# Kernel optimization log

Measured on AMD Instinct MI355X. Metric: run time of the kernel, lower is better.

## Reference

```python
import jax, jax.numpy as jnp
import numpy as np

DELTA_SCALE = 0.99
DELTA_MIN = 0.01


def setup_inputs() -> dict:
    key = jax.random.key(0)
    ks = jax.random.split(key, 6)
    B, S, Dm, N = 8, 4096, 1024, 16
    x = jax.random.normal(ks[0], (B, S, Dm), dtype=jnp.float32)
    A = jax.random.normal(ks[1], (N,), dtype=jnp.float32) * 0.1 - 1.0
    W_b = jax.random.normal(ks[2], (N, Dm), dtype=jnp.float32) / np.sqrt(Dm)
    b_b = jnp.zeros((N,), dtype=jnp.float32)
    W_c = jax.random.normal(ks[3], (Dm, N), dtype=jnp.float32) / np.sqrt(N)
    b_c = jnp.zeros((Dm,), dtype=jnp.float32)
    D = jnp.ones((Dm,), dtype=jnp.float32)
    W_t = jax.random.normal(ks[4], (1, Dm), dtype=jnp.float32) / np.sqrt(Dm)
    b_t = jnp.zeros((1,), dtype=jnp.float32)
    W_o = jax.random.normal(ks[5], (Dm, Dm), dtype=jnp.float32) / np.sqrt(Dm)
    b_o = jnp.zeros((Dm,), dtype=jnp.float32)
    return {"x": x, "A": A, "W_b": W_b, "b_b": b_b, "W_c": W_c, "b_c": b_c,
            "D": D, "W_t": W_t, "b_t": b_t, "W_o": W_o, "b_o": b_o}


def _scan_combine(left, right):
    # h_t = a_t * h_{t-1} + b_t ; compose two affine maps
    a_l, u_l = left
    a_r, u_r = right
    return (a_l * a_r, a_r * u_l + u_r)


def reference(x, A, W_b, b_b, W_c, b_c, D, W_t, b_t, W_o, b_o):
    # x: [B, S, Dm]
    delta = jax.nn.sigmoid(jnp.einsum('bsd,od->bso', x, W_t) + b_t)  # [B,S,1]
    delta = delta * DELTA_SCALE + DELTA_MIN
    Bu = jnp.einsum('bsd,nd->bsn', x, W_b) + b_b                     # [B,S,N]
    A_exp = jnp.exp(A[None, None, :] * delta)                        # [B,S,N]
    # Parallel associative scan over time: h_t = A_exp_t * h_{t-1} + Bu_t
    _, h = jax.lax.associative_scan(_scan_combine, (A_exp, Bu), axis=1)
    outputs = jnp.einsum('bsn,dn->bsd', h, W_c) + b_c                # [B,S,Dm]
    y = outputs + x * D[None, None, :]
    y = jnp.einsum('bsd,od->bso', y, W_o) + b_o                      # dropout = eval identity
    return y
```

## Files before the change

kernel.cpp:

```cpp
#include <hip/hip_runtime.h>
#include <hip/hip_bf16.h>
#include <cstdint>
#include <cstddef>

#define B_SZ 8
#define S_SZ 4096
#define DM   1024
#define NS   16
#define M_SZ (B_SZ * S_SZ)

typedef __attribute__((ext_vector_type(4))) float f32x4;
typedef __attribute__((ext_vector_type(8))) short short8;
typedef __attribute__((ext_vector_type(4))) unsigned short ushort4v;

__device__ __forceinline__ unsigned short f2bf(float f) {
  unsigned u = __float_as_uint(f);
  u += 0x7fffu + ((u >> 16) & 1u);
  return (unsigned short)(u >> 16);
}

__global__ __launch_bounds__(256) void k0_prep(
    const float* __restrict__ Wo, const float* __restrict__ D,
    const float* __restrict__ Wc, const float* __restrict__ bc,
    const float* __restrict__ bo, unsigned short* __restrict__ WoD16,
    unsigned short* __restrict__ Wco16, float* __restrict__ bz) {
  const int o = blockIdx.x;
  const int t = threadIdx.x;
  const float* wor = Wo + (size_t)o * DM;

  f32x4 wv = *(const f32x4*)(wor + t * 4);
  f32x4 dv = *(const f32x4*)(D + t * 4);
  ushort4v u;
#pragma unroll
  for (int i = 0; i < 4; ++i) u[i] = f2bf(wv[i] * dv[i]);
  *(ushort4v*)(WoD16 + (size_t)o * DM + t * 4) = u;

  const int n = t & 15, ds = t >> 4;
  float s = 0.f;
  const float* wod = wor + ds * 64;
  const float* wcd = Wc + (size_t)(ds * 64) * NS + n;
#pragma unroll 8
  for (int j = 0; j < 64; ++j) s += wod[j] * wcd[j * NS];

  f32x4 bcv = *(const f32x4*)(bc + t * 4);
  float pb = wv[0] * bcv[0] + wv[1] * bcv[1] + wv[2] * bcv[2] + wv[3] * bcv[3];

  __shared__ float red[16][17];
  __shared__ float redb[256];
  red[n][ds] = s;
  redb[t] = pb;
  __syncthreads();
  if (t < 16) {
    float acc = 0.f;
#pragma unroll
    for (int k = 0; k < 16; ++k) acc += red[t][k];
    Wco16[(size_t)o * 32 + t] = f2bf(acc);
    Wco16[(size_t)o * 32 + 16 + t] = 0;
  }
  if (t == 0) {
    float b = bo[o];
    for (int i = 0; i < 256; ++i) b += redb[i];
    bz[o] = b;
  }
}

__global__ __launch_bounds__(256) void k1_proj(
    const float* __restrict__ x, const float* __restrict__ A,
    const float* __restrict__ Wb, const float* __restrict__ bb,
    const float* __restrict__ Wt, const float* __restrict__ bt,
    float* __restrict__ Ae, float* __restrict__ Bu,
    unsigned short* __restrict__ x16) {
  __shared__ __align__(16) float Wb_s[NS * DM];
  __shared__ __align__(16) float Wt_s[DM];
  __shared__ __align__(16) float Bu_s[NS][64];
  __shared__ __align__(16) float Ae_s[NS][64];

  const int tid = threadIdx.x;
#pragma unroll
  for (int i = 0; i < 16; ++i) {
    int fi = tid * 4 + i * 1024;
    *(f32x4*)(Wb_s + fi) = *(const f32x4*)(Wb + fi);
  }
  *(f32x4*)(Wt_s + tid * 4) = *(const f32x4*)(Wt + tid * 4);

  const int lane = tid & 63;
  const int w = tid >> 6;
  const int p = lane & 15;
  const int g = lane >> 4;
  const int nlane = ((lane & 1) << 3) | (((lane >> 1) & 1) << 2) |
                    (((lane >> 2) & 1) << 1) | ((lane >> 3) & 1);
  const float a_n = A[nlane];
  const float bb_n = bb[nlane];
  const float bt0 = bt[0];

  __syncthreads();

  const int m0 = blockIdx.x * 64;
  const int b_idx = m0 >> 12;
  const int s0 = m0 & (S_SZ - 1);
  const int dq = g * 64 + p * 4;

#pragma unroll 1
  for (int grp = 0; grp < 4; ++grp) {
    const int rbase = w * 16 + grp * 4;
    f32x4 xr[4][4];
#pragma unroll
    for (int rr = 0; rr < 4; ++rr) {
      const int m = m0 + rbase + rr;
      const float* xp = x + (size_t)m * DM;
#pragma unroll
      for (int q = 0; q < 4; ++q) {
        xr[rr][q] = *(const f32x4*)(xp + q * 256 + dq);
        ushort4v xu;
#pragma unroll
        for (int e = 0; e < 4; ++e) xu[e] = f2bf(xr[rr][q][e]);
        *(ushort4v*)(x16 + (size_t)m * DM + q * 256 + dq) = xu;
      }
    }
    float bu[16][4];
#pragma unroll
    for (int n = 0; n < 16; ++n)
#pragma unroll
      for (int rr = 0; rr < 4; ++rr) bu[n][rr] = 0.f;
    float da[4] = {0.f, 0.f, 0.f, 0.f};

#pragma unroll
    for (int n = 0; n < 16; ++n) {
#pragma unroll
      for (int q = 0; q < 4; ++q) {
        f32x4 w4 = *(const f32x4*)(Wb_s + n * DM + q * 256 + dq);
#pragma unroll
        for (int e = 0; e < 4; ++e) {
#pragma unroll
          for (int rr = 0; rr < 4; ++rr) bu[n][rr] += w4[e] * xr[rr][q][e];
        }
      }
    }
#pragma unroll
    for (int q = 0; q < 4; ++q) {
      f32x4 t = *(const f32x4*)(Wt_s + q * 256 + dq);
#pragma unroll
      for (int e = 0; e < 4; ++e) {
#pragma unroll
        for (int rr = 0; rr < 4; ++rr) da[rr] += t[e] * xr[rr][q][e];
      }
    }

#pragma unroll
    for (int rr = 0; rr < 4; ++rr) {
      float v[16];
#pragma unroll
      for (int n = 0; n < 16; ++n) v[n] = bu[n][rr];
#pragma unroll
      for (int i = 0; i < 8; ++i) {
        float lo = v[i], hi = v[i + 8];
        float send = (lane & 1) ? lo : hi;
        float got = __shfl_xor(send, 1, 64);
        v[i] = ((lane & 1) ? hi : lo) + got;
      }
#pragma unroll
      for (int i = 0; i < 4; ++i) {
        float lo = v[i], hi = v[i + 4];
        float send = (lane & 2) ? lo : hi;
        float got = __shfl_xor(send, 2, 64);
        v[i] = ((lane & 2) ? hi : lo) + got;
      }
#pragma unroll
      for (int i = 0; i < 2; ++i) {
        float lo = v[i], hi = v[i + 2];
        float send = (lane & 4) ? lo : hi;
        float got = __shfl_xor(send, 4, 64);
        v[i] = ((lane & 4) ? hi : lo) + got;
      }
      {
        float lo = v[0], hi = v[1];
        float send = (lane & 8) ? lo : hi;
        float got = __shfl_xor(send, 8, 64);
        v[0] = ((lane & 8) ? hi : lo) + got;
      }
      float r = v[0];
      r += __shfl_xor(r, 16, 64);
      r += __shfl_xor(r, 32, 64);

      float dsum = da[rr];
#pragma unroll
      for (int mb = 1; mb < 64; mb <<= 1) dsum += __shfl_xor(dsum, mb, 64);
      float z = dsum + bt0;
      float delta = 1.f / (1.f + __expf(-z));
      delta = delta * 0.99f + 0.01f;

      if (lane < 16) {
        Bu_s[nlane][rbase + rr] = r + bb_n;
        Ae_s[nlane][rbase + rr] = __expf(a_n * delta);
      }
    }
  }
  __syncthreads();
  {
    int n = tid >> 4;
    int j = (tid & 15) * 4;
    size_t off = ((size_t)(b_idx * NS + n)) * S_SZ + s0 + j;
    *(f32x4*)(Bu + off) = *(const f32x4*)(&Bu_s[n][j]);
    *(f32x4*)(Ae + off) = *(const f32x4*)(&Ae_s[n][j]);
  }
}

__global__ __launch_bounds__(64) void k2_scan(const float* __restrict__ Ae,
                                              const float* __restrict__ Bu,
                                              unsigned short* __restrict__ h16) {
  const int bn = blockIdx.x;
  const int l = threadIdx.x;
  const int b = bn >> 4, n = bn & 15;
  const float* ap = Ae + (size_t)bn * S_SZ;
  const float* up = Bu + (size_t)bn * S_SZ;
  unsigned short* hp = h16 + ((size_t)b * S_SZ) * 32 + n;
  float carry = 0.f;
  float a_nx = ap[l];
  float u_nx = up[l];
#pragma unroll 1
  for (int seg = 0; seg < 64; ++seg) {
    float a = a_nx, u = u_nx;
    if (seg < 63) { a_nx = ap[(seg + 1) * 64 + l]; u_nx = up[(seg + 1) * 64 + l]; }
#pragma unroll
    for (int off = 1; off < 64; off <<= 1) {
      float aL = __shfl_up(a, off, 64);
      float uL = __shfl_up(u, off, 64);
      if (l >= off) { u = a * uL + u; a = aL * a; }
    }
    float hv = a * carry + u;
    hp[(size_t)(seg * 64 + l) * 32] = f2bf(hv);
    carry = __shfl(hv, 63, 64);
  }
}

__device__ __forceinline__ void gl_lds16(const void* g, void* l) {
  __builtin_amdgcn_global_load_lds(
      (const __attribute__((address_space(1))) void*)g,
      (__attribute__((address_space(3))) void*)l, 16, 0, 0);
}

__global__ __launch_bounds__(256) void k4_gemm(
    const unsigned short* __restrict__ x16, const unsigned short* __restrict__ h16,
    const unsigned short* __restrict__ WoD16, const unsigned short* __restrict__ Wco16,
    const float* __restrict__ bz, float* __restrict__ C) {
  __shared__ __align__(16) char smem[16384];
  const int tid = threadIdx.x;
  const int swz = (blockIdx.x & 7) * 256 + (blockIdx.x >> 3);
  const int by = swz >> 3;
  const int bx = swz & 7;
  const int lane = tid & 63;
  const int w = tid >> 6;
  const int wm = w >> 1, wn = w & 1;
  const int p = lane & 15, g = lane >> 4;

  f32x4 acc[4][4];
#pragma unroll
  for (int i = 0; i < 4; ++i)
#pragma unroll
    for (int j = 0; j < 4; ++j) acc[i][j] = (f32x4){0.f, 0.f, 0.f, 0.f};

  {
    short8 ah[4], bh[4];
#pragma unroll
    for (int mi = 0; mi < 4; ++mi)
      ah[mi] = *(const short8*)(h16 + (size_t)(by * 128 + wm * 64 + mi * 16 + p) * 32 + g * 8);
#pragma unroll
    for (int ni = 0; ni < 4; ++ni)
      bh[ni] = *(const short8*)(Wco16 + (size_t)(bx * 128 + wn * 64 + ni * 16 + p) * 32 + g * 8);
#pragma unroll
    for (int mi = 0; mi < 4; ++mi)
#pragma unroll
      for (int ni = 0; ni < 4; ++ni)
        acc[mi][ni] = __builtin_amdgcn_mfma_f32_16x16x32_bf16(ah[mi], bh[ni],
                                                              acc[mi][ni], 0, 0, 0);
  }

  const int chunk0 = tid;
  const int chunk1 = 256 + tid;
  const int rowA0 = chunk0 >> 2, colA0 = chunk0 & 3;
  const int rowA1 = chunk1 >> 2, colA1 = chunk1 & 3;
  const unsigned short* Abase = x16 + (size_t)(by * 128) * DM;
  const unsigned short* Bbase = WoD16 + (size_t)(bx * 128) * DM;

#pragma unroll 1
  for (int kk = 0; kk < 32; ++kk) {
    const int k0 = kk * 32;
    gl_lds16(Abase + (size_t)rowA0 * DM + k0 + colA0 * 8, smem + chunk0 * 16);
    gl_lds16(Abase + (size_t)rowA1 * DM + k0 + colA1 * 8, smem + chunk1 * 16);
    gl_lds16(Bbase + (size_t)rowA0 * DM + k0 + colA0 * 8, smem + 8192 + chunk0 * 16);
    gl_lds16(Bbase + (size_t)rowA1 * DM + k0 + colA1 * 8, smem + 8192 + chunk1 * 16);
    __syncthreads();

    short8 af[4], bfr[4];
#pragma unroll
    for (int mi = 0; mi < 4; ++mi)
      af[mi] = *(const short8*)(smem + (wm * 64 + mi * 16 + p) * 64 + g * 16);
#pragma unroll
    for (int ni = 0; ni < 4; ++ni)
      bfr[ni] = *(const short8*)(smem + 8192 + (wn * 64 + ni * 16 + p) * 64 + g * 16);
#pragma unroll
    for (int mi = 0; mi < 4; ++mi)
#pragma unroll
      for (int ni = 0; ni < 4; ++ni)
        acc[mi][ni] = __builtin_amdgcn_mfma_f32_16x16x32_bf16(af[mi], bfr[ni],
                                                              acc[mi][ni], 0, 0, 0);
    __syncthreads();
  }

#pragma unroll
  for (int ni = 0; ni < 4; ++ni) {
    const int c0 = bx * 128 + wn * 64 + ni * 16 + p;
    const float bzv = bz[c0];
#pragma unroll
    for (int mi = 0; mi < 4; ++mi) {
      const int r0 = by * 128 + wm * 64 + mi * 16 + g * 4;
#pragma unroll
      for (int r = 0; r < 4; ++r)
        C[(size_t)(r0 + r) * DM + c0] = acc[mi][ni][r] + bzv;
    }
  }
}

extern "C" void kernel_launch(void* const* d_in, const int* in_sizes, int n_in,
                              void* d_out, int out_size, void* d_ws, size_t ws_size,
                              hipStream_t stream) {
  const float* x  = (const float*)d_in[0];
  const float* A  = (const float*)d_in[1];
  const float* Wb = (const float*)d_in[2];
  const float* bb = (const float*)d_in[3];
  const float* Wc = (const float*)d_in[4];
  const float* bc = (const float*)d_in[5];
  const float* D  = (const float*)d_in[6];
  const float* Wt = (const float*)d_in[7];
  const float* bt = (const float*)d_in[8];
  const float* Wo = (const float*)d_in[9];
  const float* bo = (const float*)d_in[10];
  float* out = (float*)d_out;

  char* ws = (char*)d_ws;
  float* Ae = (float*)(ws);
  float* Bu = (float*)(ws + (2u << 20));
  unsigned short* WoD16 = (unsigned short*)(ws);
  unsigned short* Wco16 = (unsigned short*)(ws + (2u << 20));
  float* bz = (float*)(ws + (2u << 20) + (64u << 10));
  unsigned short* h16 = (unsigned short*)(ws + (4u << 20));
  unsigned short* x16 = (unsigned short*)(ws + (6u << 20));

  k1_proj<<<512, 256, 0, stream>>>(x, A, Wb, bb, Wt, bt, Ae, Bu, x16);
  hipMemsetAsync(h16, 0, (size_t)M_SZ * 32 * 2, stream);
  k2_scan<<<128, 64, 0, stream>>>(Ae, Bu, h16);
  k0_prep<<<1024, 256, 0, stream>>>(Wo, D, Wc, bc, bo, WoD16, Wco16, bz);
  k4_gemm<<<2048, 256, 0, stream>>>(x16, h16, WoD16, Wco16, bz, out);
}
```

Baseline: 422.2 us.

## Use MFMA for input projection, chunked parallel scan, double-buffer output GEMM

```diff
diff --git a/kernel.cpp b/kernel.cpp
--- a/kernel.cpp
+++ b/kernel.cpp
@@ -12,11 +12,45 @@
 typedef __attribute__((ext_vector_type(4))) float f32x4;
 typedef __attribute__((ext_vector_type(8))) short short8;
 typedef __attribute__((ext_vector_type(4))) unsigned short ushort4v;
+typedef __attribute__((ext_vector_type(8))) unsigned short ushort8v;
 
 __device__ __forceinline__ unsigned short f2bf(float f) {
   unsigned u = __float_as_uint(f);
   u += 0x7fffu + ((u >> 16) & 1u);
   return (unsigned short)(u >> 16);
+}
+
+__device__ __forceinline__ short8 cvt8(f32x4 a, f32x4 b) {
+  short8 r;
+  r[0] = (short)f2bf(a[0]); r[1] = (short)f2bf(a[1]);
+  r[2] = (short)f2bf(a[2]); r[3] = (short)f2bf(a[3]);
+  r[4] = (short)f2bf(b[0]); r[5] = (short)f2bf(b[1]);
+  r[6] = (short)f2bf(b[2]); r[7] = (short)f2bf(b[3]);
+  return r;
+}
+
+__device__ __forceinline__ void gl_lds16(const void* g, void* l) {
+  __builtin_amdgcn_global_load_lds(
+      (const __attribute__((address_space(1))) void*)g,
+      (__attribute__((address_space(3))) void*)l, 16, 0, 0);
+}
+
+__global__ __launch_bounds__(128) void kW(const float* __restrict__ Wb,
+                                          const float* __restrict__ Wt,
+                                          unsigned short* __restrict__ W16s) {
+  const int col = blockIdx.x;
+  const int k8 = threadIdx.x;
+  f32x4 a = {0.f, 0.f, 0.f, 0.f}, b = {0.f, 0.f, 0.f, 0.f};
+  if (col < 16) {
+    a = *(const f32x4*)(Wb + (size_t)col * DM + k8 * 8);
+    b = *(const f32x4*)(Wb + (size_t)col * DM + k8 * 8 + 4);
+  } else if (col == 16) {
+    a = *(const f32x4*)(Wt + k8 * 8);
+    b = *(const f32x4*)(Wt + k8 * 8 + 4);
+  }
+  short8 v = cvt8(a, b);
+  const int byteoff = (col * 2048 + k8 * 16) ^ ((col & 7) << 4);
+  *(short8*)((char*)W16s + byteoff) = v;
 }
 
 __global__ __launch_bounds__(256) void k0_prep(
@@ -66,184 +100,132 @@
 
 __global__ __launch_bounds__(256) void k1_proj(
     const float* __restrict__ x, const float* __restrict__ A,
-    const float* __restrict__ Wb, const float* __restrict__ bb,
-    const float* __restrict__ Wt, const float* __restrict__ bt,
+    const unsigned short* __restrict__ W16s,
+    const float* __restrict__ bb, const float* __restrict__ bt,
     float* __restrict__ Ae, float* __restrict__ Bu,
     unsigned short* __restrict__ x16) {
-  __shared__ __align__(16) float Wb_s[NS * DM];
-  __shared__ __align__(16) float Wt_s[DM];
-  __shared__ __align__(16) float Bu_s[NS][64];
-  __shared__ __align__(16) float Ae_s[NS][64];
-
-  const int tid = threadIdx.x;
-#pragma unroll
-  for (int i = 0; i < 16; ++i) {
-    int fi = tid * 4 + i * 1024;
-    *(f32x4*)(Wb_s + fi) = *(const f32x4*)(Wb + fi);
-  }
-  *(f32x4*)(Wt_s + tid * 4) = *(const f32x4*)(Wt + tid * 4);
-
-  const int lane = tid & 63;
-  const int w = tid >> 6;
-  const int p = lane & 15;
-  const int g = lane >> 4;
-  const int nlane = ((lane & 1) << 3) | (((lane >> 1) & 1) << 2) |
-                    (((lane >> 2) & 1) << 1) | ((lane >> 3) & 1);
-  const float a_n = A[nlane];
-  const float bb_n = bb[nlane];
-  const float bt0 = bt[0];
-
+  __shared__ __align__(16) char Wlds[65536];
+  __shared__ float Bu_s[16][65];
+  __shared__ float z_s[64];
+  const int tid = threadIdx.x, lane = tid & 63, w = tid >> 6;
+  const int p = lane & 15, g = lane >> 4;
+
+#pragma unroll
+  for (int i = 0; i < 16; ++i)
+    gl_lds16((const char*)W16s + (w * 16 + i) * 1024 + lane * 16,
+             Wlds + (w * 16 + i) * 1024);
   __syncthreads();
 
   const int m0 = blockIdx.x * 64;
+  const int m = m0 + w * 16 + p;
+  const float* xp = x + (size_t)m * DM;
+  unsigned short* xo = x16 + (size_t)m * DM;
+  f32x4 acc0 = {0.f, 0.f, 0.f, 0.f}, acc1 = {0.f, 0.f, 0.f, 0.f};
+  const int cb0 = p * 2048;
+  const int cb1 = (16 + p) * 2048;
+  const int sw0 = (p & 7) << 4;
+
+#pragma unroll 2
+  for (int kk = 0; kk < 32; ++kk) {
+    const int k0 = kk * 32 + g * 8;
+    f32x4 xa = *(const f32x4*)(xp + k0);
+    f32x4 xb = *(const f32x4*)(xp + k0 + 4);
+    short8 af = cvt8(xa, xb);
+    *(short8*)(xo + k0) = af;
+    const int kb = kk * 64 + g * 16;
+    short8 b0 = *(const short8*)(Wlds + ((cb0 + kb) ^ sw0));
+    short8 b1 = *(const short8*)(Wlds + ((cb1 + kb) ^ sw0));
+    acc0 = __builtin_amdgcn_mfma_f32_16x16x32_bf16(af, b0, acc0, 0, 0, 0);
+    acc1 = __builtin_amdgcn_mfma_f32_16x16x32_bf16(af, b1, acc1, 0, 0, 0);
+  }
+
+  const float bbn = bb[p];
+#pragma unroll
+  for (int r = 0; r < 4; ++r) Bu_s[p][w * 16 + g * 4 + r] = acc0[r] + bbn;
+  if (p == 0) {
+#pragma unroll
+    for (int r = 0; r < 4; ++r) z_s[w * 16 + g * 4 + r] = acc1[r];
+  }
+  __syncthreads();
+
   const int b_idx = m0 >> 12;
   const int s0 = m0 & (S_SZ - 1);
-  const int dq = g * 64 + p * 4;
-
+  const int n = tid >> 4, j0 = (tid & 15) * 4;
+  const float an = A[n];
+  const float bt0 = bt[0];
+  size_t off = ((size_t)(b_idx * NS + n)) * S_SZ + s0 + j0;
+#pragma unroll
+  for (int jj = 0; jj < 4; ++jj) {
+    float z = z_s[j0 + jj] + bt0;
+    float delta = 1.f / (1.f + __expf(-z));
+    delta = delta * 0.99f + 0.01f;
+    Ae[off + jj] = __expf(an * delta);
+    Bu[off + jj] = Bu_s[n][j0 + jj];
+  }
+}
+
+__global__ __launch_bounds__(256) void k2a(float* __restrict__ Ae, float* __restrict__ Bu,
+                                           float* __restrict__ agg_a, float* __restrict__ agg_u) {
+  const int l = threadIdx.x & 63, w = threadIdx.x >> 6;
+  const int cid = blockIdx.x * 4 + w;
+  float* ap = Ae + (size_t)cid * 256;
+  float* up = Bu + (size_t)cid * 256;
+  float ca = 1.f, cu = 0.f;
 #pragma unroll 1
-  for (int grp = 0; grp < 4; ++grp) {
-    const int rbase = w * 16 + grp * 4;
-    f32x4 xr[4][4];
-#pragma unroll
-    for (int rr = 0; rr < 4; ++rr) {
-      const int m = m0 + rbase + rr;
-      const float* xp = x + (size_t)m * DM;
-#pragma unroll
-      for (int q = 0; q < 4; ++q) {
-        xr[rr][q] = *(const f32x4*)(xp + q * 256 + dq);
-        ushort4v xu;
-#pragma unroll
-        for (int e = 0; e < 4; ++e) xu[e] = f2bf(xr[rr][q][e]);
-        *(ushort4v*)(x16 + (size_t)m * DM + q * 256 + dq) = xu;
-      }
-    }
-    float bu[16][4];
-#pragma unroll
-    for (int n = 0; n < 16; ++n)
-#pragma unroll
-      for (int rr = 0; rr < 4; ++rr) bu[n][rr] = 0.f;
-    float da[4] = {0.f, 0.f, 0.f, 0.f};
-
-#pragma unroll
-    for (int n = 0; n < 16; ++n) {
-#pragma unroll
-      for (int q = 0; q < 4; ++q) {
-        f32x4 w4 = *(const f32x4*)(Wb_s + n * DM + q * 256 + dq);
-#pragma unroll
-        for (int e = 0; e < 4; ++e) {
-#pragma unroll
-          for (int rr = 0; rr < 4; ++rr) bu[n][rr] += w4[e] * xr[rr][q][e];
-        }
-      }
-    }
-#pragma unroll
-    for (int q = 0; q < 4; ++q) {
-      f32x4 t = *(const f32x4*)(Wt_s + q * 256 + dq);
-#pragma unroll
-      for (int e = 0; e < 4; ++e) {
-#pragma unroll
-        for (int rr = 0; rr < 4; ++rr) da[rr] += t[e] * xr[rr][q][e];
-      }
-    }
-
-#pragma unroll
-    for (int rr = 0; rr < 4; ++rr) {
-      float v[16];
-#pragma unroll
-      for (int n = 0; n < 16; ++n) v[n] = bu[n][rr];
-#pragma unroll
-      for (int i = 0; i < 8; ++i) {
-        float lo = v[i], hi = v[i + 8];
-        float send = (lane & 1) ? lo : hi;
-        float got = __shfl_xor(send, 1, 64);
-        v[i] = ((lane & 1) ? hi : lo) + got;
-      }
-#pragma unroll
-      for (int i = 0; i < 4; ++i) {
-        float lo = v[i], hi = v[i + 4];
-        float send = (lane & 2) ? lo : hi;
-        float got = __shfl_xor(send, 2, 64);
-        v[i] = ((lane & 2) ? hi : lo) + got;
-      }
-#pragma unroll
-      for (int i = 0; i < 2; ++i) {
-        float lo = v[i], hi = v[i + 2];
-        float send = (lane & 4) ? lo : hi;
-        float got = __shfl_xor(send, 4, 64);
-        v[i] = ((lane & 4) ? hi : lo) + got;
-      }
-      {
-        float lo = v[0], hi = v[1];
-        float send = (lane & 8) ? lo : hi;
-        float got = __shfl_xor(send, 8, 64);
-        v[0] = ((lane & 8) ? hi : lo) + got;
-      }
-      float r = v[0];
-      r += __shfl_xor(r, 16, 64);
-      r += __shfl_xor(r, 32, 64);
-
-      float dsum = da[rr];
-#pragma unroll
-      for (int mb = 1; mb < 64; mb <<= 1) dsum += __shfl_xor(dsum, mb, 64);
-      float z = dsum + bt0;
-      float delta = 1.f / (1.f + __expf(-z));
-      delta = delta * 0.99f + 0.01f;
-
-      if (lane < 16) {
-        Bu_s[nlane][rbase + rr] = r + bb_n;
-        Ae_s[nlane][rbase + rr] = __expf(a_n * delta);
-      }
-    }
-  }
-  __syncthreads();
-  {
-    int n = tid >> 4;
-    int j = (tid & 15) * 4;
-    size_t off = ((size_t)(b_idx * NS + n)) * S_SZ + s0 + j;
-    *(f32x4*)(Bu + off) = *(const f32x4*)(&Bu_s[n][j]);
-    *(f32x4*)(Ae + off) = *(const f32x4*)(&Ae_s[n][j]);
-  }
-}
-
-__global__ __launch_bounds__(64) void k2_scan(const float* __restrict__ Ae,
-                                              const float* __restrict__ Bu,
-                                              unsigned short* __restrict__ h16) {
-  const int bn = blockIdx.x;
-  const int l = threadIdx.x;
-  const int b = bn >> 4, n = bn & 15;
-  const float* ap = Ae + (size_t)bn * S_SZ;
-  const float* up = Bu + (size_t)bn * S_SZ;
-  unsigned short* hp = h16 + ((size_t)b * S_SZ) * 32 + n;
-  float carry = 0.f;
-  float a_nx = ap[l];
-  float u_nx = up[l];
-#pragma unroll 1
-  for (int seg = 0; seg < 64; ++seg) {
-    float a = a_nx, u = u_nx;
-    if (seg < 63) { a_nx = ap[(seg + 1) * 64 + l]; u_nx = up[(seg + 1) * 64 + l]; }
+  for (int seg = 0; seg < 4; ++seg) {
+    float a = ap[seg * 64 + l], u = up[seg * 64 + l];
 #pragma unroll
     for (int off = 1; off < 64; off <<= 1) {
       float aL = __shfl_up(a, off, 64);
       float uL = __shfl_up(u, off, 64);
       if (l >= off) { u = a * uL + u; a = aL * a; }
     }
-    float hv = a * carry + u;
-    hp[(size_t)(seg * 64 + l) * 32] = f2bf(hv);
-    carry = __shfl(hv, 63, 64);
-  }
-}
-
-__device__ __forceinline__ void gl_lds16(const void* g, void* l) {
-  __builtin_amdgcn_global_load_lds(
-      (const __attribute__((address_space(1))) void*)g,
-      (__attribute__((address_space(3))) void*)l, 16, 0, 0);
+    float At = ca * a, Ut = a * cu + u;
+    ap[seg * 64 + l] = At;
+    up[seg * 64 + l] = Ut;
+    ca = __shfl(At, 63, 64);
+    cu = __shfl(Ut, 63, 64);
+  }
+  if (l == 0) { agg_a[cid] = ca; agg_u[cid] = cu; }
+}
+
+__global__ __launch_bounds__(128) void k2b(const float* __restrict__ agg_a,
+                                           const float* __restrict__ agg_u,
+                                           float* __restrict__ cpre) {
+  const int t = threadIdx.x;
+  float cu = 0.f;
+#pragma unroll
+  for (int c = 0; c < 16; ++c) {
+    cpre[t * 16 + c] = cu;
+    cu = agg_a[t * 16 + c] * cu + agg_u[t * 16 + c];
+  }
+}
+
+__global__ __launch_bounds__(256) void k2c(const float* __restrict__ Ae,
+                                           const float* __restrict__ Bu,
+                                           const float* __restrict__ cpre,
+                                           unsigned short* __restrict__ h16) {
+  const int m = blockIdx.x * 256 + threadIdx.x;
+  const int b = m >> 12, s = m & 4095, c = s >> 8;
+  unsigned short o[32];
+#pragma unroll
+  for (int n = 0; n < 16; ++n) {
+    size_t idx = ((size_t)(b * 16 + n)) * 4096 + s;
+    float h = Ae[idx] * cpre[(b * 16 + n) * 16 + c] + Bu[idx];
+    o[n] = f2bf(h);
+  }
+#pragma unroll
+  for (int n = 16; n < 32; ++n) o[n] = 0;
+  unsigned short* dst = h16 + (size_t)m * 32;
+#pragma unroll
+  for (int q = 0; q < 4; ++q) *(ushort8v*)(dst + q * 8) = *(const ushort8v*)(o + q * 8);
 }
 
 __global__ __launch_bounds__(256) void k4_gemm(
     const unsigned short* __restrict__ x16, const unsigned short* __restrict__ h16,
     const unsigned short* __restrict__ WoD16, const unsigned short* __restrict__ Wco16,
     const float* __restrict__ bz, float* __restrict__ C) {
-  __shared__ __align__(16) char smem[16384];
+  __shared__ __align__(16) char smem[32768];
   const int tid = threadIdx.x;
   const int swz = (blockIdx.x & 7) * 256 + (blockIdx.x >> 3);
   const int by = swz >> 3;
@@ -282,22 +264,30 @@
   const unsigned short* Abase = x16 + (size_t)(by * 128) * DM;
   const unsigned short* Bbase = WoD16 + (size_t)(bx * 128) * DM;
 
+#define STAGE(buf, kk)                                                              \
+  do {                                                                              \
+    char* sb = smem + (buf) * 16384;                                                \
+    const int k0_ = (kk) * 32;                                                      \
+    gl_lds16(Abase + (size_t)rowA0 * DM + k0_ + colA0 * 8, sb + chunk0 * 16);       \
+    gl_lds16(Abase + (size_t)rowA1 * DM + k0_ + colA1 * 8, sb + chunk1 * 16);       \
+    gl_lds16(Bbase + (size_t)rowA0 * DM + k0_ + colA0 * 8, sb + 8192 + chunk0 * 16);\
+    gl_lds16(Bbase + (size_t)rowA1 * DM + k0_ + colA1 * 8, sb + 8192 + chunk1 * 16);\
+  } while (0)
+
+  STAGE(0, 0);
+  __syncthreads();
+  int cur = 0;
 #pragma unroll 1
   for (int kk = 0; kk < 32; ++kk) {
-    const int k0 = kk * 32;
-    gl_lds16(Abase + (size_t)rowA0 * DM + k0 + colA0 * 8, smem + chunk0 * 16);
-    gl_lds16(Abase + (size_t)rowA1 * DM + k0 + colA1 * 8, smem + chunk1 * 16);
-    gl_lds16(Bbase + (size_t)rowA0 * DM + k0 + colA0 * 8, smem + 8192 + chunk0 * 16);
-    gl_lds16(Bbase + (size_t)rowA1 * DM + k0 + colA1 * 8, smem + 8192 + chunk1 * 16);
-    __syncthreads();
-
+    if (kk < 31) STAGE(cur ^ 1, kk + 1);
+    const char* sb = smem + cur * 16384;
     short8 af[4], bfr[4];
 #pragma unroll
     for (int mi = 0; mi < 4; ++mi)
-      af[mi] = *(const short8*)(smem + (wm * 64 + mi * 16 + p) * 64 + g * 16);
+      af[mi] = *(const short8*)(sb + (wm * 64 + mi * 16 + p) * 64 + g * 16);
 #pragma unroll
     for (int ni = 0; ni < 4; ++ni)
-      bfr[ni] = *(const short8*)(smem + 8192 + (wn * 64 + ni * 16 + p) * 64 + g * 16);
+      bfr[ni] = *(const short8*)(sb + 8192 + (wn * 64 + ni * 16 + p) * 64 + g * 16);
 #pragma unroll
     for (int mi = 0; mi < 4; ++mi)
 #pragma unroll
@@ -305,7 +295,9 @@
         acc[mi][ni] = __builtin_amdgcn_mfma_f32_16x16x32_bf16(af[mi], bfr[ni],
                                                               acc[mi][ni], 0, 0, 0);
     __syncthreads();
-  }
+    cur ^= 1;
+  }
+#undef STAGE
 
 #pragma unroll
   for (int ni = 0; ni < 4; ++ni) {
@@ -338,17 +330,23 @@
   float* out = (float*)d_out;
 
   char* ws = (char*)d_ws;
-  float* Ae = (float*)(ws);
-  float* Bu = (float*)(ws + (2u << 20));
-  unsigned short* WoD16 = (unsigned short*)(ws);
-  unsigned short* Wco16 = (unsigned short*)(ws + (2u << 20));
-  float* bz = (float*)(ws + (2u << 20) + (64u << 10));
-  unsigned short* h16 = (unsigned short*)(ws + (4u << 20));
-  unsigned short* x16 = (unsigned short*)(ws + (6u << 20));
-
-  k1_proj<<<512, 256, 0, stream>>>(x, A, Wb, bb, Wt, bt, Ae, Bu, x16);
-  hipMemsetAsync(h16, 0, (size_t)M_SZ * 32 * 2, stream);
-  k2_scan<<<128, 64, 0, stream>>>(Ae, Bu, h16);
+  float* Ae            = (float*)(ws);
+  float* Bu            = (float*)(ws + (2u << 20));
+  unsigned short* h16  = (unsigned short*)(ws + (4u << 20));
+  unsigned short* WoD16= (unsigned short*)(ws + (6u << 20));
+  unsigned short* Wco16= (unsigned short*)(ws + (8u << 20));
+  float* bz            = (float*)(ws + (8u << 20) + (64u << 10));
+  unsigned short* W16s = (unsigned short*)(ws + (8u << 20) + (68u << 10));
+  float* agg_a         = (float*)(ws + (8u << 20) + (132u << 10));
+  float* agg_u         = (float*)(ws + (8u << 20) + (140u << 10));
+  float* cpre          = (float*)(ws + (8u << 20) + (148u << 10));
+  unsigned short* x16  = (unsigned short*)(ws + (9u << 20));
+
+  kW<<<32, 128, 0, stream>>>(Wb, Wt, W16s);
   k0_prep<<<1024, 256, 0, stream>>>(Wo, D, Wc, bc, bo, WoD16, Wco16, bz);
+  k1_proj<<<512, 256, 0, stream>>>(x, A, W16s, bb, bt, Ae, Bu, x16);
+  k2a<<<512, 256, 0, stream>>>(Ae, Bu, agg_a, agg_u);
+  k2b<<<1, 128, 0, stream>>>(agg_a, agg_u, cpre);
+  k2c<<<128, 256, 0, stream>>>(Ae, Bu, cpre, h16);
   k4_gemm<<<2048, 256, 0, stream>>>(x16, h16, WoD16, Wco16, bz, out);
 }
```

Result: faster. 366.2 us (-13.3%).
